# Optimization experiments

Hardware: AMD Instinct MI355X
Metric: run time of the kernel (lower is better)

## Reference

```python
import jax, jax.numpy as jnp
import numpy as np

BS, NUM_SEG, NUM_SEN = 16, 64, 32
D_MODEL, NUM_HEAD = 1024, 8
D_K = D_MODEL // NUM_HEAD
D_FF = 2 * D_MODEL
EPS = 1e-5


def setup_inputs() -> dict:
    key = jax.random.key(0)
    ks = jax.random.split(key, 16)
    s = 1.0 / np.sqrt(D_MODEL)
    return {
        "A": jax.random.normal(ks[0], (BS, NUM_SEG, D_MODEL), jnp.float32),
        "V": jax.random.normal(ks[1], (BS, NUM_SEG, D_MODEL), jnp.float32),
        "S": jax.random.normal(ks[2], (BS, NUM_SEN, D_MODEL), jnp.float32),
        # Linear weights stored (in, out); torch y = x @ W.T + b is x @ W_io + b here.
        "Wq": jax.random.normal(ks[3], (D_MODEL, D_MODEL), jnp.float32) * s,
        "bq": jnp.zeros((D_MODEL,), jnp.float32),
        "Wk": jax.random.normal(ks[4], (D_MODEL, D_MODEL), jnp.float32) * s,
        "bk": jnp.zeros((D_MODEL,), jnp.float32),
        "Wv": jax.random.normal(ks[5], (D_MODEL, D_MODEL), jnp.float32) * s,
        "bv": jnp.zeros((D_MODEL,), jnp.float32),
        "gamma": jnp.ones((D_MODEL,), jnp.float32),
        "beta": jnp.zeros((D_MODEL,), jnp.float32),
        "W1": jax.random.normal(ks[6], (D_MODEL, D_FF), jnp.float32) * s,
        "b1": jnp.zeros((D_FF,), jnp.float32),
        "W2": jax.random.normal(ks[7], (D_FF, D_MODEL), jnp.float32) * (1.0 / np.sqrt(D_FF)),
        "b2": jnp.zeros((D_MODEL,), jnp.float32),
    }


def _layernorm(x, gamma, beta):
    mu = jnp.mean(x, axis=-1, keepdims=True)
    var = jnp.mean(jnp.square(x - mu), axis=-1, keepdims=True)
    return (x - mu) * jax.lax.rsqrt(var + EPS) * gamma + beta


def reference(A, V, S, Wq, bq, Wk, bk, Wv, bv, gamma, beta, W1, b1, W2, b2):
    bs, num_seg, d = A.shape
    num_sen = S.shape[1]
    H, dk = NUM_HEAD, D_K

    av = jnp.stack([A, V], axis=2)                      # bs, num_seg, 2, d
    v = (av @ Wv + bv).reshape(bs, 1, num_seg, 2, H, dk)
    k = (av @ Wk + bk).reshape(bs, 1, num_seg, 2, H, dk)
    Sn = _layernorm(S, gamma, beta)
    q = (Sn @ Wq + bq).reshape(bs, num_sen, 1, 1, H, dk)

    attn = jnp.sum(q * k, axis=-1, keepdims=True) / np.sqrt(dk).astype(np.float32)
    attn = jax.nn.softmax(attn, axis=-3)                # softmax over A/V modality axis (size 2)
    out = jnp.sum(attn * v, axis=-3)                    # bs, num_sen, num_seg, H, dk
    out = out.reshape(bs, num_sen, num_seg, d)

    # PositionwiseFeedForward (dropout p=0): fc2(relu(fc1(x)))
    out = jax.nn.relu(out @ W1 + b1) @ W2 + b2          # bs, num_sen, num_seg, d
    return out
```

## Files before the change

### kernel.cpp

```cpp
#include <hip/hip_runtime.h>
#include <hip/hip_bf16.h>

#define BSZ 16
#define NSEG 64
#define NSEN 32
#define DM 1024
#define NH 8
#define DKH 128
#define DFF 2048

typedef short bf16x8 __attribute__((ext_vector_type(8)));
typedef float f32x4 __attribute__((ext_vector_type(4)));

__device__ __forceinline__ float b2f(short u) {
  union { unsigned int i; float f; } c;
  c.i = ((unsigned int)(unsigned short)u) << 16;
  return c.f;
}
__device__ __forceinline__ short f2b(float f) {
  __hip_bfloat16 h = __float2bfloat16(f);
  return *reinterpret_cast<short*>(&h);
}

#define SCHED0 __builtin_amdgcn_sched_barrier(0)
#define BAR do { SCHED0; __builtin_amdgcn_s_barrier(); SCHED0; } while (0)

__global__ __launch_bounds__(256) void build_av(const float* __restrict__ A,
                                                const float* __restrict__ V,
                                                short* __restrict__ avbf) {
  int i = blockIdx.x * 256 + threadIdx.x;
  size_t o = (size_t)i * 4;
  int r = (int)(o >> 10);
  int d = (int)(o & 1023);
  int m = r & 1;
  int bseg = r >> 1;
  const float* src = (m ? V : A) + (size_t)bseg * 1024 + d;
  float4 v = *(const float4*)src;
  short4 out;
  out.x = f2b(v.x); out.y = f2b(v.y); out.z = f2b(v.z); out.w = f2b(v.w);
  *(short4*)(avbf + o) = out;
}

__global__ __launch_bounds__(256) void transpose_w(const float* __restrict__ W,
                                                   short* __restrict__ Wt,
                                                   int K, int N) {
  __shared__ float tile[32][33];
  int tx = threadIdx.x & 31, ty = threadIdx.x >> 5;
  int n0 = blockIdx.x * 32, k0 = blockIdx.y * 32;
#pragma unroll
  for (int i = 0; i < 32; i += 8)
    tile[ty + i][tx] = W[(size_t)(k0 + ty + i) * N + n0 + tx];
  __syncthreads();
#pragma unroll
  for (int i = 0; i < 32; i += 8)
    Wt[(size_t)(n0 + ty + i) * K + k0 + tx] = f2b(tile[tx][ty + i]);
}

__global__ __launch_bounds__(256) void ln_kernel(const float* __restrict__ S,
                                                 const float* __restrict__ gamma,
                                                 const float* __restrict__ beta,
                                                 short* __restrict__ Snbf) {
  int row = blockIdx.x;
  int t = threadIdx.x;
  int l = t & 63, w = t >> 6;
  const float* x = S + (size_t)row * 1024;
  float4 v = ((const float4*)x)[t];
  float s = v.x + v.y + v.z + v.w;
  __shared__ float red[4];
  __shared__ float mval, vval;
#pragma unroll
  for (int off = 32; off; off >>= 1) s += __shfl_down(s, off);
  if (l == 0) red[w] = s;
  __syncthreads();
  if (t == 0) mval = (red[0] + red[1] + red[2] + red[3]) * (1.0f / 1024.0f);
  __syncthreads();
  float mean = mval;
  float4 c = {v.x - mean, v.y - mean, v.z - mean, v.w - mean};
  float s2 = c.x * c.x + c.y * c.y + c.z * c.z + c.w * c.w;
#pragma unroll
  for (int off = 32; off; off >>= 1) s2 += __shfl_down(s2, off);
  __syncthreads();
  if (l == 0) red[w] = s2;
  __syncthreads();
  if (t == 0) vval = (red[0] + red[1] + red[2] + red[3]) * (1.0f / 1024.0f);
  __syncthreads();
  float rstd = rsqrtf(vval + 1e-5f);
  int base = t * 4;
  short4 o;
  o.x = f2b(c.x * rstd * gamma[base + 0] + beta[base + 0]);
  o.y = f2b(c.y * rstd * gamma[base + 1] + beta[base + 1]);
  o.z = f2b(c.z * rstd * gamma[base + 2] + beta[base + 2]);
  o.w = f2b(c.w * rstd * gamma[base + 3] + beta[base + 3]);
  *(short4*)(Snbf + (size_t)row * 1024 + base) = o;
}

template <int RELU, int OUTBF, int BIAS>
__global__ __launch_bounds__(256) void gemm_bf16(const short* __restrict__ Abf, int lda, long long strideA,
                                                 const short* __restrict__ Btbf, int ldb, long long strideB,
                                                 const float* __restrict__ bias,
                                                 void* __restrict__ Cout, int ldc, long long strideC,
                                                 int M, int N, int K) {
  constexpr int BM = 128, BN = 128, BK = 32;
  __shared__ short As[BM * BK];
  __shared__ short Bs[BN * BK];
  const short* Ab = Abf + (size_t)strideA * blockIdx.z;
  const short* Bb = Btbf + (size_t)strideB * blockIdx.z;

  int nwg = gridDim.x * gridDim.y;
  int L = blockIdx.y * gridDim.x + blockIdx.x;
  int bm, bn;
  if ((nwg & 7) == 0) {
    int cpx = nwg >> 3;
    int nb = (L & 7) * cpx + (L >> 3);
    bn = nb % gridDim.x;
    bm = nb / gridDim.x;
  } else {
    bn = blockIdx.x;
    bm = blockIdx.y;
  }

  const int t = threadIdx.x, w = t >> 6, l = t & 63;
  const int wm = w >> 1, wn = w & 1;
  f32x4 acc[4][4] = {};
  const size_t brow = (size_t)bm * BM, bcol = (size_t)bn * BN;

  for (int kt = 0; kt < K; kt += BK) {
#pragma unroll
    for (int i = 0; i < 2; i++) {
      int s = w * 128 + i * 64 + l;
      int row = s >> 2, c = (s & 3) * 8;
      const short* ga = Ab + (brow + row) * (size_t)lda + kt + c;
      __builtin_amdgcn_global_load_lds(
          (const __attribute__((address_space(1))) unsigned int*)ga,
          (__attribute__((address_space(3))) unsigned int*)(As + (w * 128 + i * 64) * 8),
          16, 0, 0);
      const short* gb = Bb + (bcol + row) * (size_t)ldb + kt + c;
      __builtin_amdgcn_global_load_lds(
          (const __attribute__((address_space(1))) unsigned int*)gb,
          (__attribute__((address_space(3))) unsigned int*)(Bs + (w * 128 + i * 64) * 8),
          16, 0, 0);
    }
    __syncthreads();
    bf16x8 af[4], bfr[4];
#pragma unroll
    for (int mi = 0; mi < 4; mi++)
      af[mi] = *(const bf16x8*)(As + (wm * 64 + mi * 16 + (l & 15)) * BK + (l >> 4) * 8);
#pragma unroll
    for (int ni = 0; ni < 4; ni++)
      bfr[ni] = *(const bf16x8*)(Bs + (wn * 64 + ni * 16 + (l & 15)) * BK + (l >> 4) * 8);
#pragma unroll
    for (int mi = 0; mi < 4; mi++)
#pragma unroll
      for (int ni = 0; ni < 4; ni++)
        acc[mi][ni] = __builtin_amdgcn_mfma_f32_16x16x32_bf16(af[mi], bfr[ni], acc[mi][ni], 0, 0, 0);
    __syncthreads();
  }

  const int lr = (l >> 4) * 4, lc = l & 15;
#pragma unroll
  for (int mi = 0; mi < 4; mi++) {
#pragma unroll
    for (int ni = 0; ni < 4; ni++) {
      size_t gcol = bcol + wn * 64 + ni * 16 + lc;
      float bvv = BIAS ? bias[gcol] : 0.f;
#pragma unroll
      for (int r = 0; r < 4; r++) {
        size_t grow = brow + wm * 64 + mi * 16 + lr + r;
        float val = acc[mi][ni][r] + bvv;
        if (RELU) val = fmaxf(val, 0.f);
        size_t cidx = grow * (size_t)ldc + gcol + (size_t)strideC * blockIdx.z;
        if (OUTBF)
          ((short*)Cout)[cidx] = f2b(val);
        else
          ((float*)Cout)[cidx] = val;
      }
    }
  }
}

template <int RELU, int OUTBF, int BIAS>
__global__ __launch_bounds__(512, 2) void gemm256(const short* __restrict__ Abf, int lda,
                                                  const short* __restrict__ Btbf, int ldb,
                                                  const float* __restrict__ bias,
                                                  void* __restrict__ Cout, int ldc, int K) {
  __shared__ __align__(16) short As[2][256 * 64];
  __shared__ __align__(16) short Bs[2][256 * 64];
  const int t = threadIdx.x;
  const int w = t >> 6, l = t & 63;
  const int wr = w >> 2, wc = w & 3;
  const int l15 = l & 15, lhi = l >> 4;

  int nwg = gridDim.x * gridDim.y;
  int L = blockIdx.y * gridDim.x + blockIdx.x;
  int bm, bn;
  if ((nwg & 7) == 0) {
    int cpx = nwg >> 3;
    int nb = (L & 7) * cpx + (L >> 3);
    bn = nb % gridDim.x;
    bm = nb / gridDim.x;
  } else {
    bn = blockIdx.x;
    bm = blockIdx.y;
  }
  const size_t brow = (size_t)bm * 256, bcol = (size_t)bn * 256;
  const int NT = K >> 6;

  auto stage = [&](short* dst, const short* src, int ld, size_t rowoff, int kt) {
#pragma unroll
    for (int i = 0; i < 4; ++i) {
      int seg = i * 512 + t;
      int row = seg >> 3, s = seg & 7;
      const short* g = src + (rowoff + row) * (size_t)ld + kt + ((s ^ (row & 7)) << 3);
      __builtin_amdgcn_global_load_lds(
          (const __attribute__((address_space(1))) unsigned int*)g,
          (__attribute__((address_space(3))) unsigned int*)(dst + seg * 8),
          16, 0, 0);
    }
  };
  auto rdA = [&](const short* base, int m, int kk) -> bf16x8 {
    int r = wr * 128 + m * 16 + l15;
    int d = kk * 4 + lhi;
    return *(const bf16x8*)(base + (r << 6) + ((d ^ (r & 7)) << 3));
  };
  auto rdB = [&](const short* base, int n, int kk) -> bf16x8 {
    int r = wc * 64 + n * 16 + l15;
    int d = kk * 4 + lhi;
    return *(const bf16x8*)(base + (r << 6) + ((d ^ (r & 7)) << 3));
  };

  f32x4 acc[8][4] = {};
  bf16x8 afr[4][2], bfr[4][2];

  stage(Bs[0], Btbf, ldb, bcol, 0);
  stage(As[0], Abf, lda, brow, 0);
  stage(Bs[1], Btbf, ldb, bcol, 64);
  stage(As[1], Abf, lda, brow, 64);
  asm volatile("s_waitcnt vmcnt(8)" ::: "memory");
  BAR;

  for (int T = 0; T < NT; ++T) {
    const short* Ab = As[T & 1];
    const short* Bb = Bs[T & 1];
    short* Aw = (short*)As[T & 1];
    short* Bw = (short*)Bs[T & 1];
    const int ktn = (T + 2) * 64;
    const bool st = (T + 2) < NT;

#pragma unroll
    for (int m = 0; m < 4; ++m) { afr[m][0] = rdA(Ab, m, 0); afr[m][1] = rdA(Ab, m, 1); }
#pragma unroll
    for (int n = 0; n < 2; ++n) { bfr[n][0] = rdB(Bb, n, 0); bfr[n][1] = rdB(Bb, n, 1); }
    BAR;
    __builtin_amdgcn_s_setprio(1);
#pragma unroll
    for (int m = 0; m < 4; ++m)
#pragma unroll
      for (int n = 0; n < 2; ++n) {
        acc[m][n] = __builtin_amdgcn_mfma_f32_16x16x32_bf16(afr[m][0], bfr[n][0], acc[m][n], 0, 0, 0);
        acc[m][n] = __builtin_amdgcn_mfma_f32_16x16x32_bf16(afr[m][1], bfr[n][1], acc[m][n], 0, 0, 0);
      }
    __builtin_amdgcn_s_setprio(0);
    BAR;

#pragma unroll
    for (int n = 2; n < 4; ++n) { bfr[n][0] = rdB(Bb, n, 0); bfr[n][1] = rdB(Bb, n, 1); }
    BAR;
    __builtin_amdgcn_s_setprio(1);
#pragma unroll
    for (int m = 0; m < 4; ++m)
#pragma unroll
      for (int n = 2; n < 4; ++n) {
        acc[m][n] = __builtin_amdgcn_mfma_f32_16x16x32_bf16(afr[m][0], bfr[n][0], acc[m][n], 0, 0, 0);
        acc[m][n] = __builtin_amdgcn_mfma_f32_16x16x32_bf16(afr[m][1], bfr[n][1], acc[m][n], 0, 0, 0);
      }
    __builtin_amdgcn_s_setprio(0);
    BAR;

#pragma unroll
    for (int m = 0; m < 4; ++m) { afr[m][0] = rdA(Ab, m + 4, 0); afr[m][1] = rdA(Ab, m + 4, 1); }
    if (st) stage(Bw, Btbf, ldb, bcol, ktn);
    BAR;
    __builtin_amdgcn_s_setprio(1);
#pragma unroll
    for (int m = 0; m < 4; ++m)
#pragma unroll
      for (int n = 0; n < 2; ++n) {
        acc[m + 4][n] = __builtin_amdgcn_mfma_f32_16x16x32_bf16(afr[m][0], bfr[n][0], acc[m + 4][n], 0, 0, 0);
        acc[m + 4][n] = __builtin_amdgcn_mfma_f32_16x16x32_bf16(afr[m][1], bfr[n][1], acc[m + 4][n], 0, 0, 0);
      }
    __builtin_amdgcn_s_setprio(0);
    BAR;

    if (st) stage(Aw, Abf, lda, brow, ktn);
    __builtin_amdgcn_s_setprio(1);
#pragma unroll
    for (int m = 0; m < 4; ++m)
#pragma unroll
      for (int n = 2; n < 4; ++n) {
        acc[m + 4][n] = __builtin_amdgcn_mfma_f32_16x16x32_bf16(afr[m][0], bfr[n][0], acc[m + 4][n], 0, 0, 0);
        acc[m + 4][n] = __builtin_amdgcn_mfma_f32_16x16x32_bf16(afr[m][1], bfr[n][1], acc[m + 4][n], 0, 0, 0);
      }
    __builtin_amdgcn_s_setprio(0);
    if (st) { asm volatile("s_waitcnt vmcnt(8)" ::: "memory"); }
    else    { asm volatile("s_waitcnt vmcnt(0)" ::: "memory"); }
    BAR;
  }

#pragma unroll
  for (int m = 0; m < 8; ++m) {
#pragma unroll
    for (int n = 0; n < 4; ++n) {
      size_t col = bcol + wc * 64 + n * 16 + l15;
      float bvv = BIAS ? bias[col] : 0.f;
#pragma unroll
      for (int r = 0; r < 4; ++r) {
        size_t row = brow + wr * 128 + m * 16 + lhi * 4 + r;
        float val = acc[m][n][r] + bvv;
        if (RELU) val = fmaxf(val, 0.f);
        if (OUTBF)
          ((short*)Cout)[row * (size_t)ldc + col] = f2b(val);
        else
          ((float*)Cout)[row * (size_t)ldc + col] = val;
      }
    }
  }
}

__global__ __launch_bounds__(256) void attn_p_kernel(const short* __restrict__ qbf,
                                                     const short* __restrict__ kbf,
                                                     float* __restrict__ p) {
  int blk = blockIdx.x;
  int b = blk >> 5;
  __shared__ float qs[1024];
  __shared__ float ss[1024];
  int t = threadIdx.x;
  {
    short4 qv = *(const short4*)(qbf + (size_t)blk * 1024 + t * 4);
    qs[t * 4 + 0] = b2f(qv.x);
    qs[t * 4 + 1] = b2f(qv.y);
    qs[t * 4 + 2] = b2f(qv.z);
    qs[t * 4 + 3] = b2f(qv.w);
  }
  __syncthreads();
  float sc[4];
#pragma unroll
  for (int i = 0; i < 4; i++) {
    int idx = i * 256 + t;
    int seg = idx >> 4, h = (idx >> 1) & 7, m = idx & 1;
    const short* kp = kbf + ((size_t)((b * 64 + seg) * 2 + m)) * 1024 + h * 128;
    float s = 0.f;
#pragma unroll
    for (int j = 0; j < 16; j++) {
      bf16x8 kv = *(const bf16x8*)(kp + j * 8);
#pragma unroll
      for (int e = 0; e < 8; e++) s += qs[h * 128 + j * 8 + e] * b2f(kv[e]);
    }
    sc[i] = s * 0.08838834764831845f;
  }
#pragma unroll
  for (int i = 0; i < 4; i++) ss[i * 256 + t] = sc[i];
  __syncthreads();
  for (int i = t; i < 512; i += 256) {
    float s0 = ss[2 * i], s1 = ss[2 * i + 1];
    float mx = fmaxf(s0, s1);
    float e0 = __expf(s0 - mx), e1 = __expf(s1 - mx);
    float inv = 1.f / (e0 + e1);
    int seg = i >> 3, h = i & 7;
    size_t base = (size_t)blk * 1024 + seg * 16;
    p[base + h] = e0 * inv;
    p[base + 8 + h] = e1 * inv;
  }
}

__global__ __launch_bounds__(512) void mix_kernel(const short* __restrict__ u,
                                                  const float* __restrict__ p,
                                                  const float* __restrict__ b1,
                                                  short* __restrict__ H) {
  int blk = blockIdx.x;
  int b = blk >> 6, seg = blk & 63;
  int t = threadIdx.x;
  __shared__ float ps[512];
  {
    int sen = t >> 4, j = t & 15;
    ps[t] = p[(size_t)(b * 32 + sen) * 1024 + seg * 16 + j];
  }
  int f0 = t * 4;
  float ur[16][4];
#pragma unroll
  for (int mh = 0; mh < 16; ++mh) {
    int m = mh >> 3, h = mh & 7;
    const short* up = u + ((size_t)(blk * 2 + m)) * 16384 + h * 2048 + f0;
    short4 uv = *(const short4*)up;
    ur[mh][0] = b2f(uv.x); ur[mh][1] = b2f(uv.y);
    ur[mh][2] = b2f(uv.z); ur[mh][3] = b2f(uv.w);
  }
  float4 bb = *(const float4*)(b1 + f0);
  __syncthreads();
  for (int sen = 0; sen < 32; ++sen) {
    float a0 = bb.x, a1 = bb.y, a2 = bb.z, a3 = bb.w;
#pragma unroll
    for (int mh = 0; mh < 16; ++mh) {
      float wv = ps[sen * 16 + mh];
      a0 += wv * ur[mh][0];
      a1 += wv * ur[mh][1];
      a2 += wv * ur[mh][2];
      a3 += wv * ur[mh][3];
    }
    short4 o;
    o.x = f2b(fmaxf(a0, 0.f));
    o.y = f2b(fmaxf(a1, 0.f));
    o.z = f2b(fmaxf(a2, 0.f));
    o.w = f2b(fmaxf(a3, 0.f));
    size_t row = (size_t)(b * 32 + sen) * 64 + seg;
    *(short4*)(H + row * 2048 + f0) = o;
  }
}

extern "C" void kernel_launch(void* const* d_in, const int* in_sizes, int n_in,
                              void* d_out, int out_size, void* d_ws, size_t ws_size,
                              hipStream_t stream) {
  const float* A = (const float*)d_in[0];
  const float* V = (const float*)d_in[1];
  const float* S = (const float*)d_in[2];
  const float* Wq = (const float*)d_in[3];
  const float* bq = (const float*)d_in[4];
  const float* Wk = (const float*)d_in[5];
  const float* bk = (const float*)d_in[6];
  const float* Wv = (const float*)d_in[7];
  const float* bv = (const float*)d_in[8];
  const float* gamma = (const float*)d_in[9];
  const float* beta = (const float*)d_in[10];
  const float* W1 = (const float*)d_in[11];
  const float* b1 = (const float*)d_in[12];
  const float* W2 = (const float*)d_in[13];
  const float* b2 = (const float*)d_in[14];

  const size_t MiB = 1048576;
  char* ws = (char*)d_ws;
  short* avbf = (short*)(ws + 0 * MiB);
  short* WkT  = (short*)(ws + 4 * MiB);
  short* WvT  = (short*)(ws + 6 * MiB);
  short* WqT  = (short*)(ws + 8 * MiB);
  short* W1T  = (short*)(ws + 10 * MiB);
  short* W2T  = (short*)(ws + 14 * MiB);
  short* Snbf = (short*)(ws + 18 * MiB);
  short* kbf  = (short*)(ws + 19 * MiB);
  short* vbf  = (short*)(ws + 23 * MiB);
  short* qbf  = (short*)(ws + 27 * MiB);
  float* pbuf = (float*)(ws + 28 * MiB);
  short* ubuf = (short*)(ws + 30 * MiB);
  short* Hbf  = (short*)(ws + 94 * MiB);

  build_av<<<2048, 256, 0, stream>>>(A, V, avbf);
  transpose_w<<<dim3(32, 32), 256, 0, stream>>>(Wk, WkT, 1024, 1024);
  transpose_w<<<dim3(32, 32), 256, 0, stream>>>(Wv, WvT, 1024, 1024);
  transpose_w<<<dim3(32, 32), 256, 0, stream>>>(Wq, WqT, 1024, 1024);
  transpose_w<<<dim3(64, 32), 256, 0, stream>>>(W1, W1T, 1024, 2048);
  transpose_w<<<dim3(32, 64), 256, 0, stream>>>(W2, W2T, 2048, 1024);
  ln_kernel<<<512, 256, 0, stream>>>(S, gamma, beta, Snbf);

  gemm_bf16<0, 1, 1><<<dim3(8, 16), 256, 0, stream>>>(avbf, 1024, 0, WkT, 1024, 0, bk,
                                                      kbf, 1024, 0, 2048, 1024, 1024);
  gemm_bf16<0, 1, 1><<<dim3(8, 16), 256, 0, stream>>>(avbf, 1024, 0, WvT, 1024, 0, bv,
                                                      vbf, 1024, 0, 2048, 1024, 1024);
  gemm_bf16<0, 1, 1><<<dim3(8, 4), 256, 0, stream>>>(Snbf, 1024, 0, WqT, 1024, 0, bq,
                                                     qbf, 1024, 0, 512, 1024, 1024);

  gemm_bf16<0, 1, 0><<<dim3(16, 16, 8), 256, 0, stream>>>(vbf, 1024, 128, W1T, 1024, 128, nullptr,
                                                          ubuf, 16384, 2048, 2048, 2048, 128);

  attn_p_kernel<<<512, 256, 0, stream>>>(qbf, kbf, pbuf);

  mix_kernel<<<1024, 512, 0, stream>>>(ubuf, pbuf, b1, Hbf);

  gemm256<0, 0, 1><<<dim3(4, 128), 512, 0, stream>>>(Hbf, 2048, W2T, 2048, b2,
                                                     (float*)d_out, 1024, 2048);
}
```

Measured before the change: 363.4 us.

## Restructure gemm256 prefetch pipeline and fuse K/V projection GEMMs

The large FFN2 GEMM kernel now stages the next K-tile into the alternate LDS buffer one iteration ahead. The loads are split across the four MFMA phases, and the A rows are ordered so each wave's first fragments arrive early. Fragments are register double-buffered so the next tile's first reads overlap the current tile's last MFMA block, with finer vmcnt waits. Separately, the K and V projections become one launch over a concatenated weight with a split epilogue. That fusion assumes WvT sits directly after WkT in the workspace.

```diff
diff --git a/kernel.cpp b/kernel.cpp
--- a/kernel.cpp
+++ b/kernel.cpp
@@ -94,11 +94,14 @@
   *(short4*)(Snbf + (size_t)row * 1024 + base) = o;
 }
 
-template <int RELU, int OUTBF, int BIAS>
+template <int RELU, int OUTBF, int BIAS, int SPLIT>
 __global__ __launch_bounds__(256) void gemm_bf16(const short* __restrict__ Abf, int lda, long long strideA,
                                                  const short* __restrict__ Btbf, int ldb, long long strideB,
                                                  const float* __restrict__ bias,
-                                                 void* __restrict__ Cout, int ldc, long long strideC,
+                                                 const float* __restrict__ bias2,
+                                                 void* __restrict__ Cout,
+                                                 void* __restrict__ Cout2,
+                                                 int ldc, long long strideC,
                                                  int M, int N, int K) {
   constexpr int BM = 128, BN = 128, BK = 32;
   __shared__ short As[BM * BK];
@@ -162,17 +165,21 @@
 #pragma unroll
     for (int ni = 0; ni < 4; ni++) {
       size_t gcol = bcol + wn * 64 + ni * 16 + lc;
-      float bvv = BIAS ? bias[gcol] : 0.f;
+      int half = SPLIT ? (gcol >= 1024) : 0;
+      size_t cc = SPLIT ? (gcol - (half ? 1024 : 0)) : gcol;
+      const float* bp = (SPLIT && half) ? bias2 : bias;
+      void* op = (SPLIT && half) ? Cout2 : Cout;
+      float bvv = BIAS ? bp[cc] : 0.f;
 #pragma unroll
       for (int r = 0; r < 4; r++) {
         size_t grow = brow + wm * 64 + mi * 16 + lr + r;
         float val = acc[mi][ni][r] + bvv;
         if (RELU) val = fmaxf(val, 0.f);
-        size_t cidx = grow * (size_t)ldc + gcol + (size_t)strideC * blockIdx.z;
+        size_t cidx = grow * (size_t)ldc + cc + (size_t)strideC * blockIdx.z;
         if (OUTBF)
-          ((short*)Cout)[cidx] = f2b(val);
+          ((short*)op)[cidx] = f2b(val);
         else
-          ((float*)Cout)[cidx] = val;
+          ((float*)op)[cidx] = val;
       }
     }
   }
@@ -205,17 +212,14 @@
   const size_t brow = (size_t)bm * 256, bcol = (size_t)bn * 256;
   const int NT = K >> 6;
 
-  auto stage = [&](short* dst, const short* src, int ld, size_t rowoff, int kt) {
-#pragma unroll
-    for (int i = 0; i < 4; ++i) {
-      int seg = i * 512 + t;
-      int row = seg >> 3, s = seg & 7;
-      const short* g = src + (rowoff + row) * (size_t)ld + kt + ((s ^ (row & 7)) << 3);
-      __builtin_amdgcn_global_load_lds(
-          (const __attribute__((address_space(1))) unsigned int*)g,
-          (__attribute__((address_space(3))) unsigned int*)(dst + seg * 8),
-          16, 0, 0);
-    }
+  auto stage1 = [&](short* dst, const short* src, int ld, size_t rowoff, int kt, int r) {
+    int seg = r * 512 + t;
+    int row = seg >> 3, s = seg & 7;
+    const short* g = src + (rowoff + row) * (size_t)ld + kt + ((s ^ (row & 7)) << 3);
+    __builtin_amdgcn_global_load_lds(
+        (const __attribute__((address_space(1))) unsigned int*)g,
+        (__attribute__((address_space(3))) unsigned int*)(dst + seg * 8),
+        16, 0, 0);
   };
   auto rdA = [&](const short* base, int m, int kk) -> bf16x8 {
     int r = wr * 128 + m * 16 + l15;
@@ -229,80 +233,105 @@
   };
 
   f32x4 acc[8][4] = {};
-  bf16x8 afr[4][2], bfr[4][2];
-
-  stage(Bs[0], Btbf, ldb, bcol, 0);
-  stage(As[0], Abf, lda, brow, 0);
-  stage(Bs[1], Btbf, ldb, bcol, 64);
-  stage(As[1], Abf, lda, brow, 64);
-  asm volatile("s_waitcnt vmcnt(8)" ::: "memory");
+  bf16x8 afr0[4][2], afr2[4][2], bfr1[2][2], bfr2[2][2];
+
+  stage1(Bs[0], Btbf, ldb, bcol, 0, 0);
+  stage1(Bs[0], Btbf, ldb, bcol, 0, 1);
+  stage1(Bs[0], Btbf, ldb, bcol, 0, 2);
+  stage1(Bs[0], Btbf, ldb, bcol, 0, 3);
+  stage1(As[0], Abf, lda, brow, 0, 0);
+  stage1(As[0], Abf, lda, brow, 0, 2);
+  stage1(As[0], Abf, lda, brow, 0, 1);
+  stage1(As[0], Abf, lda, brow, 0, 3);
+  asm volatile("s_waitcnt vmcnt(2)" ::: "memory");
   BAR;
+#pragma unroll
+  for (int m = 0; m < 4; ++m) { afr0[m][0] = rdA(As[0], m, 0); afr0[m][1] = rdA(As[0], m, 1); }
+#pragma unroll
+  for (int n = 0; n < 2; ++n) { bfr1[n][0] = rdB(Bs[0], n, 0); bfr1[n][1] = rdB(Bs[0], n, 1); }
 
   for (int T = 0; T < NT; ++T) {
-    const short* Ab = As[T & 1];
-    const short* Bb = Bs[T & 1];
-    short* Aw = (short*)As[T & 1];
-    short* Bw = (short*)Bs[T & 1];
-    const int ktn = (T + 2) * 64;
-    const bool st = (T + 2) < NT;
-
-#pragma unroll
-    for (int m = 0; m < 4; ++m) { afr[m][0] = rdA(Ab, m, 0); afr[m][1] = rdA(Ab, m, 1); }
-#pragma unroll
-    for (int n = 0; n < 2; ++n) { bfr[n][0] = rdB(Bb, n, 0); bfr[n][1] = rdB(Bb, n, 1); }
+    const int buf = T & 1, nxt = buf ^ 1;
+    const short* Ab = As[buf];
+    const short* Bb = Bs[buf];
+    short* Aw = (short*)As[nxt];
+    short* Bw = (short*)Bs[nxt];
+    const int ktn = (T + 1) * 64;
+    const bool st = (T + 1) < NT;
+
+    if (st) {
+      stage1(Bw, Btbf, ldb, bcol, ktn, 0);
+      stage1(Bw, Btbf, ldb, bcol, ktn, 1);
+      stage1(Bw, Btbf, ldb, bcol, ktn, 2);
+      stage1(Bw, Btbf, ldb, bcol, ktn, 3);
+    }
+#pragma unroll
+    for (int n = 0; n < 2; ++n) { bfr2[n][0] = rdB(Bb, n + 2, 0); bfr2[n][1] = rdB(Bb, n + 2, 1); }
     BAR;
     __builtin_amdgcn_s_setprio(1);
 #pragma unroll
     for (int m = 0; m < 4; ++m)
 #pragma unroll
       for (int n = 0; n < 2; ++n) {
-        acc[m][n] = __builtin_amdgcn_mfma_f32_16x16x32_bf16(afr[m][0], bfr[n][0], acc[m][n], 0, 0, 0);
-        acc[m][n] = __builtin_amdgcn_mfma_f32_16x16x32_bf16(afr[m][1], bfr[n][1], acc[m][n], 0, 0, 0);
+        acc[m][n] = __builtin_amdgcn_mfma_f32_16x16x32_bf16(afr0[m][0], bfr1[n][0], acc[m][n], 0, 0, 0);
+        acc[m][n] = __builtin_amdgcn_mfma_f32_16x16x32_bf16(afr0[m][1], bfr1[n][1], acc[m][n], 0, 0, 0);
       }
     __builtin_amdgcn_s_setprio(0);
-    BAR;
-
-#pragma unroll
-    for (int n = 2; n < 4; ++n) { bfr[n][0] = rdB(Bb, n, 0); bfr[n][1] = rdB(Bb, n, 1); }
+    if (st) { asm volatile("s_waitcnt vmcnt(4)" ::: "memory"); }
+    else    { asm volatile("s_waitcnt vmcnt(0)" ::: "memory"); }
+    BAR;
+
+    if (st) {
+      stage1(Aw, Abf, lda, brow, ktn, 0);
+      stage1(Aw, Abf, lda, brow, ktn, 2);
+    }
+#pragma unroll
+    for (int m = 0; m < 4; ++m) { afr2[m][0] = rdA(Ab, m + 4, 0); afr2[m][1] = rdA(Ab, m + 4, 1); }
     BAR;
     __builtin_amdgcn_s_setprio(1);
 #pragma unroll
     for (int m = 0; m < 4; ++m)
 #pragma unroll
-      for (int n = 2; n < 4; ++n) {
-        acc[m][n] = __builtin_amdgcn_mfma_f32_16x16x32_bf16(afr[m][0], bfr[n][0], acc[m][n], 0, 0, 0);
-        acc[m][n] = __builtin_amdgcn_mfma_f32_16x16x32_bf16(afr[m][1], bfr[n][1], acc[m][n], 0, 0, 0);
+      for (int n = 0; n < 2; ++n) {
+        acc[m][n + 2] = __builtin_amdgcn_mfma_f32_16x16x32_bf16(afr0[m][0], bfr2[n][0], acc[m][n + 2], 0, 0, 0);
+        acc[m][n + 2] = __builtin_amdgcn_mfma_f32_16x16x32_bf16(afr0[m][1], bfr2[n][1], acc[m][n + 2], 0, 0, 0);
       }
     __builtin_amdgcn_s_setprio(0);
     BAR;
 
-#pragma unroll
-    for (int m = 0; m < 4; ++m) { afr[m][0] = rdA(Ab, m + 4, 0); afr[m][1] = rdA(Ab, m + 4, 1); }
-    if (st) stage(Bw, Btbf, ldb, bcol, ktn);
+    if (st) {
+      stage1(Aw, Abf, lda, brow, ktn, 1);
+      stage1(Aw, Abf, lda, brow, ktn, 3);
+    }
     BAR;
     __builtin_amdgcn_s_setprio(1);
 #pragma unroll
     for (int m = 0; m < 4; ++m)
 #pragma unroll
       for (int n = 0; n < 2; ++n) {
-        acc[m + 4][n] = __builtin_amdgcn_mfma_f32_16x16x32_bf16(afr[m][0], bfr[n][0], acc[m + 4][n], 0, 0, 0);
-        acc[m + 4][n] = __builtin_amdgcn_mfma_f32_16x16x32_bf16(afr[m][1], bfr[n][1], acc[m + 4][n], 0, 0, 0);
+        acc[m + 4][n] = __builtin_amdgcn_mfma_f32_16x16x32_bf16(afr2[m][0], bfr1[n][0], acc[m + 4][n], 0, 0, 0);
+        acc[m + 4][n] = __builtin_amdgcn_mfma_f32_16x16x32_bf16(afr2[m][1], bfr1[n][1], acc[m + 4][n], 0, 0, 0);
       }
     __builtin_amdgcn_s_setprio(0);
-    BAR;
-
-    if (st) stage(Aw, Abf, lda, brow, ktn);
+    asm volatile("s_waitcnt vmcnt(2)" ::: "memory");
+    BAR;
+
+    if (st) {
+#pragma unroll
+      for (int m = 0; m < 4; ++m) { afr0[m][0] = rdA(Aw, m, 0); afr0[m][1] = rdA(Aw, m, 1); }
+#pragma unroll
+      for (int n = 0; n < 2; ++n) { bfr1[n][0] = rdB(Bw, n, 0); bfr1[n][1] = rdB(Bw, n, 1); }
+    }
+    BAR;
     __builtin_amdgcn_s_setprio(1);
 #pragma unroll
     for (int m = 0; m < 4; ++m)
 #pragma unroll
-      for (int n = 2; n < 4; ++n) {
-        acc[m + 4][n] = __builtin_amdgcn_mfma_f32_16x16x32_bf16(afr[m][0], bfr[n][0], acc[m + 4][n], 0, 0, 0);
-        acc[m + 4][n] = __builtin_amdgcn_mfma_f32_16x16x32_bf16(afr[m][1], bfr[n][1], acc[m + 4][n], 0, 0, 0);
+      for (int n = 0; n < 2; ++n) {
+        acc[m + 4][n + 2] = __builtin_amdgcn_mfma_f32_16x16x32_bf16(afr2[m][0], bfr2[n][0], acc[m + 4][n + 2], 0, 0, 0);
+        acc[m + 4][n + 2] = __builtin_amdgcn_mfma_f32_16x16x32_bf16(afr2[m][1], bfr2[n][1], acc[m + 4][n + 2], 0, 0, 0);
       }
     __builtin_amdgcn_s_setprio(0);
-    if (st) { asm volatile("s_waitcnt vmcnt(8)" ::: "memory"); }
-    else    { asm volatile("s_waitcnt vmcnt(0)" ::: "memory"); }
     BAR;
   }
 
@@ -459,15 +488,16 @@
   transpose_w<<<dim3(32, 64), 256, 0, stream>>>(W2, W2T, 2048, 1024);
   ln_kernel<<<512, 256, 0, stream>>>(S, gamma, beta, Snbf);
 
-  gemm_bf16<0, 1, 1><<<dim3(8, 16), 256, 0, stream>>>(avbf, 1024, 0, WkT, 1024, 0, bk,
-                                                      kbf, 1024, 0, 2048, 1024, 1024);
-  gemm_bf16<0, 1, 1><<<dim3(8, 16), 256, 0, stream>>>(avbf, 1024, 0, WvT, 1024, 0, bv,
-                                                      vbf, 1024, 0, 2048, 1024, 1024);
-  gemm_bf16<0, 1, 1><<<dim3(8, 4), 256, 0, stream>>>(Snbf, 1024, 0, WqT, 1024, 0, bq,
-                                                     qbf, 1024, 0, 512, 1024, 1024);
-
-  gemm_bf16<0, 1, 0><<<dim3(16, 16, 8), 256, 0, stream>>>(vbf, 1024, 128, W1T, 1024, 128, nullptr,
-                                                          ubuf, 16384, 2048, 2048, 2048, 128);
+  gemm_bf16<0, 1, 1, 1><<<dim3(16, 16), 256, 0, stream>>>(avbf, 1024, 0, WkT, 1024, 0,
+                                                          bk, bv, kbf, vbf, 1024, 0,
+                                                          2048, 2048, 1024);
+  gemm_bf16<0, 1, 1, 0><<<dim3(8, 4), 256, 0, stream>>>(Snbf, 1024, 0, WqT, 1024, 0,
+                                                        bq, nullptr, qbf, nullptr, 1024, 0,
+                                                        512, 1024, 1024);
+
+  gemm_bf16<0, 1, 0, 0><<<dim3(16, 16, 8), 256, 0, stream>>>(vbf, 1024, 128, W1T, 1024, 128,
+                                                             nullptr, nullptr, ubuf, nullptr,
+                                                             16384, 2048, 2048, 2048, 128);
 
   attn_p_kernel<<<512, 256, 0, stream>>>(qbf, kbf, pbuf);
 
```

Measured after the change: 390.1 us. 1.07x slower.

## Merge preprocessing kernels and fuse K/V/Q projection GEMMs into single launches

Applied to the files above, without the earlier changes.

Seven preprocessing launches (bf16 cast of A/V, five weight transposes, layernorm) become one block-indexed prep kernel. The K, V and Q projection GEMMs become one kernel of 288 blocks. K and V are computed as one N=2048 GEMM, relying on WkT and WvT sitting next to each other in the workspace (4 MiB and 6 MiB). The aim is to cut launch overhead and fill more CUs per launch, but the new GEMM is a simpler single-buffered loop that may run slower than the earlier template GEMM.

```diff
diff --git a/kernel.cpp b/kernel.cpp
--- a/kernel.cpp
+++ b/kernel.cpp
@@ -25,73 +25,177 @@
 #define SCHED0 __builtin_amdgcn_sched_barrier(0)
 #define BAR do { SCHED0; __builtin_amdgcn_s_barrier(); SCHED0; } while (0)
 
-__global__ __launch_bounds__(256) void build_av(const float* __restrict__ A,
-                                                const float* __restrict__ V,
-                                                short* __restrict__ avbf) {
-  int i = blockIdx.x * 256 + threadIdx.x;
-  size_t o = (size_t)i * 4;
-  int r = (int)(o >> 10);
-  int d = (int)(o & 1023);
-  int m = r & 1;
-  int bseg = r >> 1;
-  const float* src = (m ? V : A) + (size_t)bseg * 1024 + d;
-  float4 v = *(const float4*)src;
-  short4 out;
-  out.x = f2b(v.x); out.y = f2b(v.y); out.z = f2b(v.z); out.w = f2b(v.w);
-  *(short4*)(avbf + o) = out;
-}
-
-__global__ __launch_bounds__(256) void transpose_w(const float* __restrict__ W,
-                                                   short* __restrict__ Wt,
-                                                   int K, int N) {
-  __shared__ float tile[32][33];
+__device__ __forceinline__ void transpose_body(const float* __restrict__ W,
+                                               short* __restrict__ Wt,
+                                               int K, int N, int bx, int by,
+                                               float* tile ) {
   int tx = threadIdx.x & 31, ty = threadIdx.x >> 5;
-  int n0 = blockIdx.x * 32, k0 = blockIdx.y * 32;
+  int n0 = bx * 32, k0 = by * 32;
 #pragma unroll
   for (int i = 0; i < 32; i += 8)
-    tile[ty + i][tx] = W[(size_t)(k0 + ty + i) * N + n0 + tx];
+    tile[(ty + i) * 33 + tx] = W[(size_t)(k0 + ty + i) * N + n0 + tx];
   __syncthreads();
 #pragma unroll
   for (int i = 0; i < 32; i += 8)
-    Wt[(size_t)(n0 + ty + i) * K + k0 + tx] = f2b(tile[tx][ty + i]);
-}
-
-__global__ __launch_bounds__(256) void ln_kernel(const float* __restrict__ S,
-                                                 const float* __restrict__ gamma,
-                                                 const float* __restrict__ beta,
-                                                 short* __restrict__ Snbf) {
-  int row = blockIdx.x;
+    Wt[(size_t)(n0 + ty + i) * K + k0 + tx] = f2b(tile[tx * 33 + ty + i]);
+}
+
+__global__ __launch_bounds__(256) void prep_kernel(
+    const float* __restrict__ A, const float* __restrict__ V, short* __restrict__ avbf,
+    const float* __restrict__ Wk, short* __restrict__ WkT,
+    const float* __restrict__ Wv, short* __restrict__ WvT,
+    const float* __restrict__ Wq, short* __restrict__ WqT,
+    const float* __restrict__ W1, short* __restrict__ W1T,
+    const float* __restrict__ W2, short* __restrict__ W2T,
+    const float* __restrict__ S, const float* __restrict__ gamma,
+    const float* __restrict__ beta, short* __restrict__ Snbf) {
+  __shared__ float smem[32 * 33];
+  int bid = blockIdx.x;
   int t = threadIdx.x;
-  int l = t & 63, w = t >> 6;
-  const float* x = S + (size_t)row * 1024;
-  float4 v = ((const float4*)x)[t];
-  float s = v.x + v.y + v.z + v.w;
-  __shared__ float red[4];
-  __shared__ float mval, vval;
-#pragma unroll
-  for (int off = 32; off; off >>= 1) s += __shfl_down(s, off);
-  if (l == 0) red[w] = s;
-  __syncthreads();
-  if (t == 0) mval = (red[0] + red[1] + red[2] + red[3]) * (1.0f / 1024.0f);
-  __syncthreads();
-  float mean = mval;
-  float4 c = {v.x - mean, v.y - mean, v.z - mean, v.w - mean};
-  float s2 = c.x * c.x + c.y * c.y + c.z * c.z + c.w * c.w;
-#pragma unroll
-  for (int off = 32; off; off >>= 1) s2 += __shfl_down(s2, off);
-  __syncthreads();
-  if (l == 0) red[w] = s2;
-  __syncthreads();
-  if (t == 0) vval = (red[0] + red[1] + red[2] + red[3]) * (1.0f / 1024.0f);
-  __syncthreads();
-  float rstd = rsqrtf(vval + 1e-5f);
-  int base = t * 4;
-  short4 o;
-  o.x = f2b(c.x * rstd * gamma[base + 0] + beta[base + 0]);
-  o.y = f2b(c.y * rstd * gamma[base + 1] + beta[base + 1]);
-  o.z = f2b(c.z * rstd * gamma[base + 2] + beta[base + 2]);
-  o.w = f2b(c.w * rstd * gamma[base + 3] + beta[base + 3]);
-  *(short4*)(Snbf + (size_t)row * 1024 + base) = o;
+  if (bid < 2048) {
+    int i = bid * 256 + t;
+    size_t o = (size_t)i * 4;
+    int r = (int)(o >> 10);
+    int d = (int)(o & 1023);
+    int m = r & 1;
+    int bseg = r >> 1;
+    const float* src = (m ? V : A) + (size_t)bseg * 1024 + d;
+    float4 v = *(const float4*)src;
+    short4 out;
+    out.x = f2b(v.x); out.y = f2b(v.y); out.z = f2b(v.z); out.w = f2b(v.w);
+    *(short4*)(avbf + o) = out;
+  } else if (bid < 3072) {
+    int id = bid - 2048;
+    transpose_body(Wk, WkT, 1024, 1024, id & 31, id >> 5, smem);
+  } else if (bid < 4096) {
+    int id = bid - 3072;
+    transpose_body(Wv, WvT, 1024, 1024, id & 31, id >> 5, smem);
+  } else if (bid < 5120) {
+    int id = bid - 4096;
+    transpose_body(Wq, WqT, 1024, 1024, id & 31, id >> 5, smem);
+  } else if (bid < 7168) {
+    int id = bid - 5120;
+    transpose_body(W1, W1T, 1024, 2048, id & 63, id >> 6, smem);
+  } else if (bid < 9216) {
+    int id = bid - 7168;
+    transpose_body(W2, W2T, 2048, 1024, id & 31, id >> 5, smem);
+  } else {
+    int row = bid - 9216;
+    int l = t & 63, w = t >> 6;
+    const float* x = S + (size_t)row * 1024;
+    float4 v = ((const float4*)x)[t];
+    float s = v.x + v.y + v.z + v.w;
+#pragma unroll
+    for (int off = 32; off; off >>= 1) s += __shfl_down(s, off);
+    if (l == 0) smem[w] = s;
+    __syncthreads();
+    if (t == 0) smem[4] = (smem[0] + smem[1] + smem[2] + smem[3]) * (1.0f / 1024.0f);
+    __syncthreads();
+    float mean = smem[4];
+    float4 c = {v.x - mean, v.y - mean, v.z - mean, v.w - mean};
+    float s2 = c.x * c.x + c.y * c.y + c.z * c.z + c.w * c.w;
+#pragma unroll
+    for (int off = 32; off; off >>= 1) s2 += __shfl_down(s2, off);
+    __syncthreads();
+    if (l == 0) smem[w] = s2;
+    __syncthreads();
+    if (t == 0) smem[5] = (smem[0] + smem[1] + smem[2] + smem[3]) * (1.0f / 1024.0f);
+    __syncthreads();
+    float rstd = rsqrtf(smem[5] + 1e-5f);
+    int base = t * 4;
+    short4 o;
+    o.x = f2b(c.x * rstd * gamma[base + 0] + beta[base + 0]);
+    o.y = f2b(c.y * rstd * gamma[base + 1] + beta[base + 1]);
+    o.z = f2b(c.z * rstd * gamma[base + 2] + beta[base + 2]);
+    o.w = f2b(c.w * rstd * gamma[base + 3] + beta[base + 3]);
+    *(short4*)(Snbf + (size_t)row * 1024 + base) = o;
+  }
+}
+
+__global__ __launch_bounds__(256) void gemm_kvq(const short* __restrict__ avbf,
+                                                const short* __restrict__ WkvT,
+                                                const float* __restrict__ bk,
+                                                const float* __restrict__ bv,
+                                                short* __restrict__ kbf,
+                                                short* __restrict__ vbf,
+                                                const short* __restrict__ Snbf,
+                                                const short* __restrict__ WqT,
+                                                const float* __restrict__ bq,
+                                                short* __restrict__ qbf) {
+  constexpr int BK = 32;
+  __shared__ short As[128 * BK];
+  __shared__ short Bs[128 * BK];
+  int bid = blockIdx.x;
+  const short *Ab, *Bb;
+  const float *biasLo, *biasHi;
+  short *Clo, *Chi;
+  int bm, bn;
+  bool split;
+  if (bid < 256) {
+    int nb = (bid & 7) * 32 + (bid >> 3);
+    bn = nb & 15; bm = nb >> 4;
+    Ab = avbf; Bb = WkvT; biasLo = bk; biasHi = bv; Clo = kbf; Chi = vbf; split = true;
+  } else {
+    int id = bid - 256;
+    bm = id >> 3; bn = id & 7;
+    Ab = Snbf; Bb = WqT; biasLo = bq; biasHi = bq; Clo = qbf; Chi = qbf; split = false;
+  }
+
+  const int t = threadIdx.x, w = t >> 6, l = t & 63;
+  const int wm = w >> 1, wn = w & 1;
+  f32x4 acc[4][4] = {};
+  const size_t brow = (size_t)bm * 128, bcol = (size_t)bn * 128;
+
+  for (int kt = 0; kt < 1024; kt += BK) {
+#pragma unroll
+    for (int i = 0; i < 2; i++) {
+      int s = w * 128 + i * 64 + l;
+      int row = s >> 2, c = (s & 3) * 8;
+      const short* ga = Ab + (brow + row) * (size_t)1024 + kt + c;
+      __builtin_amdgcn_global_load_lds(
+          (const __attribute__((address_space(1))) unsigned int*)ga,
+          (__attribute__((address_space(3))) unsigned int*)(As + (w * 128 + i * 64) * 8),
+          16, 0, 0);
+      const short* gb = Bb + (bcol + row) * (size_t)1024 + kt + c;
+      __builtin_amdgcn_global_load_lds(
+          (const __attribute__((address_space(1))) unsigned int*)gb,
+          (__attribute__((address_space(3))) unsigned int*)(Bs + (w * 128 + i * 64) * 8),
+          16, 0, 0);
+    }
+    __syncthreads();
+    bf16x8 af[4], bfr[4];
+#pragma unroll
+    for (int mi = 0; mi < 4; mi++)
+      af[mi] = *(const bf16x8*)(As + (wm * 64 + mi * 16 + (l & 15)) * BK + (l >> 4) * 8);
+#pragma unroll
+    for (int ni = 0; ni < 4; ni++)
+      bfr[ni] = *(const bf16x8*)(Bs + (wn * 64 + ni * 16 + (l & 15)) * BK + (l >> 4) * 8);
+#pragma unroll
+    for (int mi = 0; mi < 4; mi++)
+#pragma unroll
+      for (int ni = 0; ni < 4; ni++)
+        acc[mi][ni] = __builtin_amdgcn_mfma_f32_16x16x32_bf16(af[mi], bfr[ni], acc[mi][ni], 0, 0, 0);
+    __syncthreads();
+  }
+
+  const int lr = (l >> 4) * 4, lc = l & 15;
+#pragma unroll
+  for (int mi = 0; mi < 4; mi++) {
+#pragma unroll
+    for (int ni = 0; ni < 4; ni++) {
+      size_t gcol = bcol + wn * 64 + ni * 16 + lc;
+      int half = split ? (gcol >= 1024) : 0;
+      size_t cc = half ? (gcol - 1024) : gcol;
+      const float* bp = half ? biasHi : biasLo;
+      short* op = half ? Chi : Clo;
+      float bvv = bp[cc];
+#pragma unroll
+      for (int r = 0; r < 4; r++) {
+        size_t grow = brow + wm * 64 + mi * 16 + lr + r;
+        op[grow * 1024 + cc] = f2b(acc[mi][ni][r] + bvv);
+      }
+    }
+  }
 }
 
 template <int RELU, int OUTBF, int BIAS>
@@ -451,23 +555,14 @@
   short* ubuf = (short*)(ws + 30 * MiB);
   short* Hbf  = (short*)(ws + 94 * MiB);
 
-  build_av<<<2048, 256, 0, stream>>>(A, V, avbf);
-  transpose_w<<<dim3(32, 32), 256, 0, stream>>>(Wk, WkT, 1024, 1024);
-  transpose_w<<<dim3(32, 32), 256, 0, stream>>>(Wv, WvT, 1024, 1024);
-  transpose_w<<<dim3(32, 32), 256, 0, stream>>>(Wq, WqT, 1024, 1024);
-  transpose_w<<<dim3(64, 32), 256, 0, stream>>>(W1, W1T, 1024, 2048);
-  transpose_w<<<dim3(32, 64), 256, 0, stream>>>(W2, W2T, 2048, 1024);
-  ln_kernel<<<512, 256, 0, stream>>>(S, gamma, beta, Snbf);
-
-  gemm_bf16<0, 1, 1><<<dim3(8, 16), 256, 0, stream>>>(avbf, 1024, 0, WkT, 1024, 0, bk,
-                                                      kbf, 1024, 0, 2048, 1024, 1024);
-  gemm_bf16<0, 1, 1><<<dim3(8, 16), 256, 0, stream>>>(avbf, 1024, 0, WvT, 1024, 0, bv,
-                                                      vbf, 1024, 0, 2048, 1024, 1024);
-  gemm_bf16<0, 1, 1><<<dim3(8, 4), 256, 0, stream>>>(Snbf, 1024, 0, WqT, 1024, 0, bq,
-                                                     qbf, 1024, 0, 512, 1024, 1024);
-
-  gemm_bf16<0, 1, 0><<<dim3(16, 16, 8), 256, 0, stream>>>(vbf, 1024, 128, W1T, 1024, 128, nullptr,
-                                                          ubuf, 16384, 2048, 2048, 2048, 128);
+  prep_kernel<<<9728, 256, 0, stream>>>(A, V, avbf, Wk, WkT, Wv, WvT, Wq, WqT,
+                                        W1, W1T, W2, W2T, S, gamma, beta, Snbf);
+
+  gemm_kvq<<<288, 256, 0, stream>>>(avbf, WkT, bk, bv, kbf, vbf, Snbf, WqT, bq, qbf);
+
+  gemm_bf16<0, 1, 0><<<dim3(16, 16, 8), 256, 0, stream>>>(vbf, 1024, 128, W1T, 1024, 128,
+                                                          nullptr, ubuf, 16384, 2048,
+                                                          2048, 2048, 128);
 
   attn_p_kernel<<<512, 256, 0, stream>>>(qbf, kbf, pbuf);
 
```

Result: faster. 301.9 us (-16.9%).
